# Performance work log

Hardware: AMD Instinct MI355X
Metric: run time of the kernel (lower is better)

## Reference

```python
import jax, jax.numpy as jnp
import numpy as np

N = 50000      # nodes
E = 500000     # edges
D = 128        # model dim (in_dim == out_dim)
H = 8          # heads
DH = D // H    # head dim = 16
BN_EPS = 1e-5
Z_EPS = 1e-6


def setup_inputs() -> dict:
    key = jax.random.key(0)
    ks = jax.random.split(key, 24)
    w = lambda k, shape, s=0.05: (jax.random.normal(k, shape, jnp.float32) * s)
    inp = {}
    inp['v'] = jax.random.normal(ks[0], (N, D), jnp.float32)
    inp['e'] = jax.random.normal(ks[1], (E, D), jnp.float32)
    inp['envelope'] = jax.random.uniform(ks[2], (E, 1, 1), jnp.float32)
    inp['src'] = jax.random.randint(ks[3], (E,), 0, N, jnp.int32)
    inp['dst'] = jax.random.randint(ks[4], (E,), 0, N, jnp.int32)
    # attention projections (use_bias=False)
    inp['WQ'] = w(ks[5], (D, D)); inp['WK'] = w(ks[6], (D, D))
    inp['WV'] = w(ks[7], (D, D)); inp['We'] = w(ks[8], (D, D))
    # output projections
    inp['WO_v'] = w(ks[9], (D, D)); inp['bO_v'] = jnp.zeros((D,), jnp.float32)
    inp['WO_e'] = w(ks[10], (D, D)); inp['bO_e'] = jnp.zeros((D,), jnp.float32)
    # batch-norm affine params
    inp['g1_v'] = jnp.ones((D,), jnp.float32); inp['b1_v'] = jnp.zeros((D,), jnp.float32)
    inp['g1_e'] = jnp.ones((D,), jnp.float32); inp['b1_e'] = jnp.zeros((D,), jnp.float32)
    inp['g2_v'] = jnp.ones((D,), jnp.float32); inp['b2_v'] = jnp.zeros((D,), jnp.float32)
    inp['g2_e'] = jnp.ones((D,), jnp.float32); inp['b2_e'] = jnp.zeros((D,), jnp.float32)
    # FFN weights (hidden = 2*D)
    inp['W1v'] = w(ks[11], (D, 2 * D)); inp['b1v'] = jnp.zeros((2 * D,), jnp.float32)
    inp['W2v'] = w(ks[12], (2 * D, D)); inp['b2v'] = jnp.zeros((D,), jnp.float32)
    inp['W1e'] = w(ks[13], (D, 2 * D)); inp['b1e'] = jnp.zeros((2 * D,), jnp.float32)
    inp['W2e'] = w(ks[14], (2 * D, D)); inp['b2e'] = jnp.zeros((D,), jnp.float32)
    return inp


def _batchnorm(x, g, b):
    # BatchNorm1d in training mode: biased batch stats over axis 0
    m = x.mean(0)
    var = x.var(0)
    return (x - m) * jax.lax.rsqrt(var + BN_EPS) * g + b


def _forward(v, e, envelope, src, dst,
             WQ, WK, WV, We, WO_v, bO_v, WO_e, bO_e,
             g1_v, b1_v, g1_e, b1_e,
             W1v, b1v, W2v, b2v, W1e, b1e, W2e, b2e,
             g2_v, b2_v, g2_e, b2_e):
    # --- multi-head edge attention ---
    Q = (v @ WQ).reshape(N, H, DH)
    K = (v @ WK).reshape(N, H, DH)
    V = (v @ WV).reshape(N, H, DH)
    pe = (e @ We).reshape(E, H, DH)
    # score = K[src] * Q[dst] / sqrt(Dh) * proj_e   (elementwise, per head)
    score = K[src] * Q[dst] / np.sqrt(DH).astype(np.float32) * pe  # [E,H,Dh]
    e_attn = score.reshape(E, D)                                    # e_out
    s = jnp.exp(jnp.clip(score.sum(-1, keepdims=True), -5.0, 5.0))  # [E,H,1]
    msg = V[src] * envelope * s                                     # [E,H,Dh]
    wV = jax.ops.segment_sum(msg, dst, num_segments=N)              # [N,H,Dh]
    z = jax.ops.segment_sum(s, dst, num_segments=N)                 # [N,H,1]
    v_attn = (wV / (z + Z_EPS)).reshape(N, D)
    # --- O projection + residual + batchnorm ---
    v1 = _batchnorm(v + (v_attn @ WO_v + bO_v), g1_v, b1_v)
    e1 = _batchnorm(e + (e_attn @ WO_e + bO_e), g1_e, b1_e)
    # --- FFN + residual + batchnorm ---
    v2 = _batchnorm(v1 + (jax.nn.relu(v1 @ W1v + b1v) @ W2v + b2v), g2_v, b2_v)
    e2 = _batchnorm(e1 + (jax.nn.relu(e1 @ W1e + b1e) @ W2e + b2e), g2_e, b2_e)
    return v2, e2


def reference(v, e, envelope, src, dst,
              WQ, WK, WV, We, WO_v, bO_v, WO_e, bO_e,
              g1_v, b1_v, g1_e, b1_e,
              W1v, b1v, W2v, b2v, W1e, b1e, W2e, b2e,
              g2_v, b2_v, g2_e, b2_e):
    return _forward(v, e, envelope, src, dst,
                    WQ, WK, WV, We, WO_v, bO_v, WO_e, bO_e,
                    g1_v, b1_v, g1_e, b1_e,
                    W1v, b1v, W2v, b2v, W1e, b1e, W2e, b2e,
                    g2_v, b2_v, g2_e, b2_e)
```

## Files before the change

### kernel.cpp

```cpp
#include <hip/hip_runtime.h>
#include <hip/hip_bf16.h>

#define N_NODES 50000
#define N_EDGES 500000
#define DIM 128
#define RSTRIDE 256

typedef __bf16 bf16_t;
typedef __bf16 bf16x8 __attribute__((ext_vector_type(8)));
typedef __bf16 bf16x4 __attribute__((ext_vector_type(4)));
typedef __bf16 bf16x2 __attribute__((ext_vector_type(2)));
typedef float f32x4 __attribute__((ext_vector_type(4)));

#define MFMA(a,b,c) __builtin_amdgcn_mfma_f32_16x16x32_bf16((a),(b),(c),0,0,0)

__device__ __forceinline__ int swz(int row, int kbyte){ return kbyte ^ ((row & 7) << 4); }
__device__ __forceinline__ int hswz(int row, int kbyte){ return kbyte ^ ((row & 15) << 4); }

__device__ __forceinline__ bf16x8 lds_frag(const char* s, int row, int rowb, int kbyte){
  return *(const bf16x8*)(s + row * rowb + swz(row, kbyte));
}

__device__ __forceinline__ void copy16(char* dst, const char* __restrict__ src, int bytes){
  for (int o = threadIdx.x * 16; o < bytes; o += blockDim.x * 16)
    *(f32x4*)(dst + o) = *(const f32x4*)(src + o);
}

struct WPrep {
  const float* w[10];
  int Kd[10], Nd[10], off[10], cum[10], mode[10];
};

__global__ void k_wprep(WPrep d, char* img, int total){
  for (int idx = blockIdx.x * blockDim.x + threadIdx.x; idx < total; idx += gridDim.x * blockDim.x){
    int i = 0;
#pragma unroll
    for (int j = 1; j < 10; j++) if (idx >= d.cum[j]) i = j;
    int loc = idx - d.cum[i];
    int K = d.Kd[i], N = d.Nd[i];
    int n = loc / K, k = loc - n * K;
    float val = d.w[i][(size_t)k * N + n];
    int nn = n;
    if (d.mode[i] == 1) nn = ((n & 7) << 4) | (n >> 3);
    if (d.mode[i] == 3) nn = ((n & 15) << 4) | (n >> 4);
    *(bf16_t*)(img + d.off[i] + nn * (K * 2) + swz(nn, k * 2)) = (bf16_t)val;
  }
}

__global__ void k_count(const int* __restrict__ dst, int* __restrict__ cnt){
  int i = blockIdx.x * blockDim.x + threadIdx.x;
  if (i < N_EDGES) atomicAdd(&cnt[dst[i]], 1);
}

__global__ __launch_bounds__(1024) void k_scan(const int* __restrict__ cnt,
                                               int* __restrict__ rowptr, int* __restrict__ wp){
  __shared__ int wsum[16];
  __shared__ int wpre[16];
  __shared__ int scarry;
  const int tid = threadIdx.x, lane = tid & 63, wv = tid >> 6;
  if (tid == 0) scarry = 0;
  for (int base = 0; base < N_NODES; base += 8192){
    int i0 = base + tid * 8;
    int v[8], p[8];
    int tsum = 0;
#pragma unroll
    for (int j = 0; j < 8; j++){
      int idx = i0 + j;
      v[j] = (idx < N_NODES) ? cnt[idx] : 0;
      p[j] = tsum; tsum += v[j];
    }
    int x = tsum;
#pragma unroll
    for (int off = 1; off < 64; off <<= 1){
      int t = __shfl_up(x, off);
      if (lane >= off) x += t;
    }
    if (lane == 63) wsum[wv] = x;
    __syncthreads();
    if (tid == 0){
      int run = scarry;
#pragma unroll
      for (int j = 0; j < 16; j++){ int t = wsum[j]; wpre[j] = run; run += t; }
      scarry = run;
    }
    __syncthreads();
    int texcl = wpre[wv] + x - tsum;
#pragma unroll
    for (int j = 0; j < 8; j++){
      int idx = i0 + j;
      if (idx < N_NODES){ rowptr[idx] = texcl + p[j]; wp[idx] = texcl + p[j]; }
    }
    __syncthreads();
  }
  if (tid == 0) rowptr[N_NODES] = scarry;
}

__global__ void k_fill(const int* __restrict__ dst, int* __restrict__ wp, int* __restrict__ csr){
  int i = blockIdx.x * blockDim.x + threadIdx.x;
  if (i < N_EDGES){
    int p = atomicAdd(&wp[dst[i]], 1);
    csr[p] = i;
  }
}

__global__ __launch_bounds__(512) void k_qkv(
    const float* __restrict__ v, const char* __restrict__ img,
    bf16_t* __restrict__ Q, bf16_t* __restrict__ K, bf16_t* __restrict__ V, int M)
{
  __shared__ __align__(16) char sm[65536];
  char* sX = sm;
  char* sW = sm + 32768;
  const int tid = threadIdx.x, lane = tid & 63, wave = tid >> 6;
  const int r0 = blockIdx.x * 128;
  for (int c = tid; c < 2048; c += 512){
    int row = c >> 4, kc = c & 15, grow = r0 + row;
    float f[8];
    if (grow < M){
      const float4* p = (const float4*)(v + (size_t)grow * DIM + kc * 8);
      float4 u0 = p[0], u1 = p[1];
      f[0]=u0.x; f[1]=u0.y; f[2]=u0.z; f[3]=u0.w;
      f[4]=u1.x; f[5]=u1.y; f[6]=u1.z; f[7]=u1.w;
    } else {
#pragma unroll
      for (int j=0;j<8;j++) f[j] = 0.f;
    }
    bf16x8 o;
#pragma unroll
    for (int j=0;j<8;j++) o[j] = (bf16_t)f[j];
    *(bf16x8*)(sX + row * 256 + swz(row, kc * 16)) = o;
  }
  const int rowA = wave * 16 + (lane & 15);
  const int kb0 = (lane >> 4) * 16;
  const int crow = wave*16 + (lane >> 4)*4;
  const int ccol = lane & 15;
  const f32x4 zero4 = {0.f, 0.f, 0.f, 0.f};
#pragma unroll
  for (int w3 = 0; w3 < 3; w3++){
    __syncthreads();
    copy16(sW, img + w3 * 32768, 32768);
    __syncthreads();
    f32x4 acc[8];
#pragma unroll
    for (int b=0;b<8;b++) acc[b] = zero4;
#pragma unroll
    for (int ks=0; ks<4; ks++){
      bf16x8 a = lds_frag(sX, rowA, 256, ks*64 + kb0);
#pragma unroll
      for (int nt=0; nt<8; nt++){
        int rn = nt*16 + (lane & 15);
        bf16x8 b = lds_frag(sW, rn, 256, ks*64 + kb0);
        acc[nt] = MFMA(a, b, acc[nt]);
      }
    }
    bf16_t* o = (w3 == 0) ? Q : ((w3 == 1) ? K : V);
#pragma unroll
    for (int r=0; r<4; r++){
      int grow = r0 + crow + r;
      if (grow < M){
        bf16x8 t;
#pragma unroll
        for (int nt=0; nt<8; nt++) t[nt] = (bf16_t)acc[nt][r];
        *(bf16x8*)(o + (size_t)grow * DIM + ccol*8) = t;
      }
    }
  }
}

__global__ __launch_bounds__(512, 4) void k_edge(
    const float* __restrict__ e,
    const int* __restrict__ src, const int* __restrict__ dst,
    const bf16_t* __restrict__ Qb, const bf16_t* __restrict__ Kb,
    const char* __restrict__ imgWe, const char* __restrict__ imgWo,
    const float* __restrict__ bOe,
    bf16_t* __restrict__ e1_pre, float* __restrict__ sv,
    float* __restrict__ stats, int M)
{
  __shared__ __align__(16) char sm[33792];
  char* sBuf = sm;
  float* sStats = (float*)(sm + 32768);
  const int tid = threadIdx.x, lane = tid & 63, wave = tid >> 6;
  const int r0 = blockIdx.x * 128;
  const int q = lane >> 4, ccol = lane & 15;
  const int crow = wave*16 + q*4;
  const int rowA = wave*16 + ccol;
  const int kb0 = q * 16;
  bf16x8 Kg[4], Qg[4];
#pragma unroll
  for (int r=0;r<4;r++){
    int ed = r0 + crow + r; if (ed >= M) ed = M - 1;
    int sn = src[ed], dn = dst[ed];
    Kg[r] = *(const bf16x8*)(Kb + (size_t)sn * DIM + ccol * 8);
    Qg[r] = *(const bf16x8*)(Qb + (size_t)dn * DIM + ccol * 8);
  }
  int grA = r0 + rowA; if (grA >= M) grA = M - 1;
  const f32x4* epA = (const f32x4*)(e + (size_t)grA * DIM);
  f32x4 ea[8];
#pragma unroll
  for (int ks=0; ks<4; ks++){
    ea[2*ks]   = epA[ks*8 + q*2];
    ea[2*ks+1] = epA[ks*8 + q*2 + 1];
  }
  copy16(sBuf, imgWe, 32768);
  bf16x8 eAb[4];
#pragma unroll
  for (int ks=0; ks<4; ks++){
#pragma unroll
    for (int j=0;j<4;j++){
      eAb[ks][j]   = (bf16_t)ea[2*ks][j];
      eAb[ks][4+j] = (bf16_t)ea[2*ks+1][j];
    }
  }
  __syncthreads();
  const f32x4 zero4 = {0.f,0.f,0.f,0.f};
  f32x4 pe[8];
#pragma unroll
  for (int i=0;i<8;i++) pe[i] = zero4;
#pragma unroll
  for (int ks=0; ks<4; ks++){
#pragma unroll
    for (int nt=0; nt<8; nt++){
      bf16x8 b = lds_frag(sBuf, nt*16 + ccol, 256, ks*64 + kb0);
      pe[nt] = MFMA(eAb[ks], b, pe[nt]);
    }
  }
  __syncthreads();
#pragma unroll
  for (int r=0;r<4;r++){
    int row = crow + r;
    bf16x8 t;
    float hsum = 0.f;
#pragma unroll
    for (int nt=0; nt<8; nt++){
      float sc = pe[nt][r] * 0.25f * (float)Kg[r][nt] * (float)Qg[r][nt];
      t[nt] = (bf16_t)sc;
      hsum += sc;
    }
    *(bf16x8*)(sBuf + row*256 + swz(row, ccol*16)) = t;
    float ts = hsum + __shfl_xor(hsum, 1);
    int ed = r0 + row;
    if (!(ccol & 1) && ed < M)
      sv[(size_t)ed*8 + (ccol >> 1)] = __expf(fminf(5.f, fmaxf(-5.f, ts)));
  }
  bf16x8 w2a[4];
#pragma unroll
  for (int ks=0; ks<4; ks++)
    w2a[ks] = *(const bf16x8*)(imgWo + rowA*256 + swz(rowA, ks*64 + kb0));
  __syncthreads();
  f32x4 a2[8];
#pragma unroll
  for (int i=0;i<8;i++) a2[i] = zero4;
#pragma unroll
  for (int ks=0; ks<4; ks++){
#pragma unroll
    for (int nt=0; nt<8; nt++){
      bf16x8 b = lds_frag(sBuf, nt*16 + ccol, 256, ks*64 + kb0);
      a2[nt] = MFMA(w2a[ks], b, a2[nt]);
    }
  }
  float4 bo = *(const float4*)(bOe + crow);
  float s1[4] = {0.f,0.f,0.f,0.f}, s2[4] = {0.f,0.f,0.f,0.f};
#pragma unroll
  for (int nt=0; nt<8; nt++){
    int erow = r0 + nt*16 + ccol;
    int gr = (erow < M) ? erow : (M - 1);
    f32x4 er = *(const f32x4*)(e + (size_t)gr*DIM + crow);
    float val[4];
    val[0] = a2[nt][0] + er[0] + bo.x;
    val[1] = a2[nt][1] + er[1] + bo.y;
    val[2] = a2[nt][2] + er[2] + bo.z;
    val[3] = a2[nt][3] + er[3] + bo.w;
    if (erow < M){
      bf16x4 t;
#pragma unroll
      for (int r=0;r<4;r++) t[r] = (bf16_t)val[r];
      *(bf16x4*)(e1_pre + (size_t)erow*RSTRIDE + crow) = t;
    } else {
#pragma unroll
      for (int r=0;r<4;r++) val[r] = 0.f;
    }
#pragma unroll
    for (int r=0;r<4;r++){ s1[r] += val[r]; s2[r] += val[r]*val[r]; }
  }
#pragma unroll
  for (int r=0;r<4;r++){
    s1[r] += __shfl_xor(s1[r], 1); s1[r] += __shfl_xor(s1[r], 2);
    s1[r] += __shfl_xor(s1[r], 4); s1[r] += __shfl_xor(s1[r], 8);
    s2[r] += __shfl_xor(s2[r], 1); s2[r] += __shfl_xor(s2[r], 2);
    s2[r] += __shfl_xor(s2[r], 4); s2[r] += __shfl_xor(s2[r], 8);
  }
  if (ccol == 0){
#pragma unroll
    for (int r=0;r<4;r++){
      sStats[crow + r] = s1[r];
      sStats[128 + crow + r] = s2[r];
    }
  }
  __syncthreads();
  if (tid < 256) unsafeAtomicAdd(&stats[tid], sStats[tid]);
}

__global__ __launch_bounds__(512) void k_agg(
    const int* __restrict__ rowptr, const int* __restrict__ csr,
    const int* __restrict__ src, const float* __restrict__ envl,
    const float* __restrict__ sv, const bf16_t* __restrict__ V,
    bf16_t* __restrict__ vAttn, int M)
{
  const int wave = threadIdx.x >> 6, lane = threadIdx.x & 63;
  const int n = blockIdx.x * 8 + wave;
  if (n >= M) return;
  const int beg = rowptr[n], end = rowptr[n + 1];
  const int h = lane >> 3;
  float ax = 0.f, ay = 0.f, zacc = 0.f;
  int i = beg;
  for (; i + 4 <= end; i += 4){
    int e0 = csr[i], e1 = csr[i+1], e2 = csr[i+2], e3 = csr[i+3];
    int sn0 = src[e0], sn1 = src[e1], sn2 = src[e2], sn3 = src[e3];
    float sv0 = sv[(size_t)e0*8 + h], sv1 = sv[(size_t)e1*8 + h];
    float sv2 = sv[(size_t)e2*8 + h], sv3 = sv[(size_t)e3*8 + h];
    float n0 = envl[e0], n1 = envl[e1], n2 = envl[e2], n3 = envl[e3];
    bf16x2 a0 = *(const bf16x2*)(V + (size_t)sn0 * DIM + lane * 2);
    bf16x2 a1 = *(const bf16x2*)(V + (size_t)sn1 * DIM + lane * 2);
    bf16x2 a2v = *(const bf16x2*)(V + (size_t)sn2 * DIM + lane * 2);
    bf16x2 a3 = *(const bf16x2*)(V + (size_t)sn3 * DIM + lane * 2);
    float w0 = n0*sv0, w1 = n1*sv1, w2 = n2*sv2, w3 = n3*sv3;
    ax += (float)a0[0]*w0 + (float)a1[0]*w1 + (float)a2v[0]*w2 + (float)a3[0]*w3;
    ay += (float)a0[1]*w0 + (float)a1[1]*w1 + (float)a2v[1]*w2 + (float)a3[1]*w3;
    zacc += sv0 + sv1 + sv2 + sv3;
  }
  for (; i < end; i++){
    int eid = csr[i];
    int sn = src[eid];
    float s = sv[(size_t)eid * 8 + h];
    float env = envl[eid];
    const bf16x2 vv = *(const bf16x2*)(V + (size_t)sn * DIM + lane * 2);
    float w = env * s;
    ax += (float)vv[0] * w; ay += (float)vv[1] * w;
    zacc += s;
  }
  float inv = 1.f / (zacc + 1e-6f);
  bf16x2 o; o[0] = (bf16_t)(ax * inv); o[1] = (bf16_t)(ay * inv);
  *(bf16x2*)(vAttn + (size_t)n * DIM + lane * 2) = o;
}

__global__ __launch_bounds__(512) void k_nodeout(
    const bf16_t* __restrict__ vAttn, const float* __restrict__ v,
    const char* __restrict__ imgWo, const float* __restrict__ bOv,
    bf16_t* __restrict__ v1_pre, float* __restrict__ stats, int M)
{
  __shared__ __align__(16) char sm[66560];
  char* sW = sm;
  char* sX = sm + 32768;
  float* sStats = (float*)(sm + 65536);
  const int tid = threadIdx.x, lane = tid & 63, wave = tid >> 6;
  const int r0 = blockIdx.x * 128;
  copy16(sW, imgWo, 32768);
  if (tid < 256) sStats[tid] = 0.f;
  for (int c = tid; c < 2048; c += 512){
    int row = c >> 4, kc = c & 15, grow = r0 + row;
    bf16x8 o;
    if (grow < M){
      o = *(const bf16x8*)(vAttn + (size_t)grow * DIM + kc * 8);
    } else {
#pragma unroll
      for (int j=0;j<8;j++) o[j] = (bf16_t)0.f;
    }
    *(bf16x8*)(sX + row*256 + swz(row, kc*16)) = o;
  }
  __syncthreads();
  const int rowA = wave*16 + (lane & 15);
  const int kb0 = (lane >> 4)*16;
  const f32x4 zero4 = {0.f,0.f,0.f,0.f};
  f32x4 acc[8];
#pragma unroll
  for (int i=0;i<8;i++) acc[i]=zero4;
#pragma unroll
  for (int ks=0;ks<4;ks++){
    bf16x8 a = lds_frag(sX, rowA, 256, ks*64+kb0);
#pragma unroll
    for (int nt=0;nt<8;nt++){
      int rn = nt*16 + (lane&15);
      bf16x8 b = lds_frag(sW, rn, 256, ks*64+kb0);
      acc[nt] = MFMA(a,b,acc[nt]);
    }
  }
  const int crow = wave*16 + (lane>>4)*4;
  const int ccol = lane & 15;
  float4 bo0 = *(const float4*)(bOv + ccol*8);
  float4 bo1 = *(const float4*)(bOv + ccol*8 + 4);
  float s1[8], s2[8];
#pragma unroll
  for (int j=0;j<8;j++){ s1[j]=0.f; s2[j]=0.f; }
#pragma unroll
  for (int r=0;r<4;r++){
    int grow = r0 + crow + r;
    float val[8];
    if (grow < M){
      const float4* vp = (const float4*)(v + (size_t)grow*DIM + ccol*8);
      float4 v0 = vp[0], v1 = vp[1];
      val[0]=acc[0][r]+v0.x+bo0.x; val[1]=acc[1][r]+v0.y+bo0.y;
      val[2]=acc[2][r]+v0.z+bo0.z; val[3]=acc[3][r]+v0.w+bo0.w;
      val[4]=acc[4][r]+v1.x+bo1.x; val[5]=acc[5][r]+v1.y+bo1.y;
      val[6]=acc[6][r]+v1.z+bo1.z; val[7]=acc[7][r]+v1.w+bo1.w;
      bf16x8 t;
#pragma unroll
      for (int j=0;j<8;j++) t[j] = (bf16_t)val[j];
      *(bf16x8*)(v1_pre + (size_t)grow*RSTRIDE + ccol*8) = t;
    } else {
#pragma unroll
      for (int j=0;j<8;j++) val[j]=0.f;
    }
#pragma unroll
    for (int j=0;j<8;j++){ s1[j] += val[j]; s2[j] += val[j]*val[j]; }
  }
#pragma unroll
  for (int j=0;j<8;j++){
    s1[j] += __shfl_xor(s1[j], 16); s1[j] += __shfl_xor(s1[j], 32);
    s2[j] += __shfl_xor(s2[j], 16); s2[j] += __shfl_xor(s2[j], 32);
  }
  if (lane < 16){
#pragma unroll
    for (int j=0;j<8;j++){
      atomicAdd(&sStats[ccol*8 + j], s1[j]);
      atomicAdd(&sStats[128 + ccol*8 + j], s2[j]);
    }
  }
  __syncthreads();
  if (tid < 256) unsafeAtomicAdd(&stats[tid], sStats[tid]);
}

struct FinArgs { const float* st; const float* g; const float* b; float* ss; float invM; };

__global__ void k_finstats(FinArgs a0, FinArgs a1){
  FinArgs a = (blockIdx.x == 0) ? a0 : a1;
  int c = threadIdx.x;
  float mean = a.st[c] * a.invM;
  float var  = a.st[128 + c] * a.invM - mean * mean;
  float scl  = a.g[c] * rsqrtf(var + 1e-5f);
  a.ss[c] = scl;
  a.ss[128 + c] = a.b[c] - mean * scl;
}

__global__ __launch_bounds__(512, 4) void k_ffn(
    bf16_t* __restrict__ xio, const float* __restrict__ ss1,
    const char* __restrict__ img1, const float* __restrict__ b1,
    const char* __restrict__ img2, const float* __restrict__ b2,
    float* __restrict__ stats2, int M)
{
  __shared__ __align__(16) char sm[66560];
  char* sA = sm;
  char* sB = sm + 32768;
  float* sStats = (float*)(sm + 65536);
  const int tid = threadIdx.x, lane = tid & 63, wave = tid >> 6;
  const int r0 = blockIdx.x * 128;
  const int rowA = wave*16 + (lane & 15);
  const int q = lane >> 4;
  const int kb0 = q * 16;
  const int crow = wave*16 + q*4;
  const int ccol = lane & 15;
  const f32x4 zero4 = {0.f,0.f,0.f,0.f};

  float4 sc0 = *(const float4*)(ss1 + ccol*8);
  float4 sc1 = *(const float4*)(ss1 + ccol*8 + 4);
  float4 sh0 = *(const float4*)(ss1 + 128 + ccol*8);
  float4 sh1 = *(const float4*)(ss1 + 128 + ccol*8 + 4);
  const float4* bq = (const float4*)(b1 + ccol * 16);
  float4 bq0 = bq[0], bq1 = bq[1], bq2 = bq[2], bq3 = bq[3];

  copy16(sB, img1, 32768);
  if (tid < 256) sStats[tid] = 0.f;
  int grA = r0 + rowA; if (grA >= M) grA = M - 1;
  const bf16_t* xrow = xio + (size_t)grA * RSTRIDE;
  bf16x8 araw[4];
#pragma unroll
  for (int ks=0; ks<4; ks++)
    araw[ks] = *(const bf16x8*)(xrow + ks*32 + q*8);
  bf16x8 xres[4];
#pragma unroll
  for (int r = 0; r < 4; r++){
    int grow = r0 + crow + r;
    bf16x8 o;
    if (grow < M){
      bf16x8 u = *(const bf16x8*)(xio + (size_t)grow*RSTRIDE + ccol*8);
      o[0]=(bf16_t)((float)u[0]*sc0.x+sh0.x); o[1]=(bf16_t)((float)u[1]*sc0.y+sh0.y);
      o[2]=(bf16_t)((float)u[2]*sc0.z+sh0.z); o[3]=(bf16_t)((float)u[3]*sc0.w+sh0.w);
      o[4]=(bf16_t)((float)u[4]*sc1.x+sh1.x); o[5]=(bf16_t)((float)u[5]*sc1.y+sh1.y);
      o[6]=(bf16_t)((float)u[6]*sc1.z+sh1.z); o[7]=(bf16_t)((float)u[7]*sc1.w+sh1.w);
    } else {
#pragma unroll
      for (int j=0;j<8;j++) o[j]=(bf16_t)0.f;
    }
    xres[r] = o;
  }
  bf16x8 xAb[4];
#pragma unroll
  for (int ks=0; ks<4; ks++){
    const f32x4* sp = (const f32x4*)(ss1 + ks*32 + q*8);
    const f32x4* hp = (const f32x4*)(ss1 + 128 + ks*32 + q*8);
    f32x4 s0 = sp[0], s1v = sp[1], h0 = hp[0], h1 = hp[1];
#pragma unroll
    for (int j=0;j<4;j++){
      xAb[ks][j]   = (bf16_t)((float)araw[ks][j]  *s0[j]  + h0[j]);
      xAb[ks][4+j] = (bf16_t)((float)araw[ks][4+j]*s1v[j] + h1[j]);
    }
  }
  __syncthreads();

  bf16x8 hreg[8];
  f32x4 wbuf[4];

#pragma unroll
  for (int i=0;i<4;i++) wbuf[i] = *(const f32x4*)(img1 + 32768 + tid*16 + i*8192);
  {
    f32x4 acc[8];
#pragma unroll
    for (int i=0;i<8;i++) acc[i]=zero4;
#pragma unroll
    for (int ks=0;ks<4;ks++){
#pragma unroll
      for (int nt=0;nt<8;nt++){
        int rn = nt*16 + (lane&15);
        bf16x8 b = lds_frag(sB, rn, 256, ks*64+kb0);
        acc[nt] = MFMA(xAb[ks], b, acc[nt]);
      }
    }
#pragma unroll
    for (int r=0;r<4;r++){
      bf16x8 t;
      t[0]=(bf16_t)fmaxf(acc[0][r]+bq0.x,0.f); t[1]=(bf16_t)fmaxf(acc[1][r]+bq0.y,0.f);
      t[2]=(bf16_t)fmaxf(acc[2][r]+bq0.z,0.f); t[3]=(bf16_t)fmaxf(acc[3][r]+bq0.w,0.f);
      t[4]=(bf16_t)fmaxf(acc[4][r]+bq1.x,0.f); t[5]=(bf16_t)fmaxf(acc[5][r]+bq1.y,0.f);
      t[6]=(bf16_t)fmaxf(acc[6][r]+bq1.z,0.f); t[7]=(bf16_t)fmaxf(acc[7][r]+bq1.w,0.f);
      hreg[r] = t;
    }
  }
  __syncthreads();
#pragma unroll
  for (int i=0;i<4;i++) *(f32x4*)(sB + tid*16 + i*8192) = wbuf[i];
  __syncthreads();
#pragma unroll
  for (int i=0;i<4;i++){
    int o = tid*16 + i*8192;
    wbuf[i] = *(const f32x4*)(img2 + (o >> 8)*512 + (o & 255));
  }
  {
    f32x4 acc[8];
#pragma unroll
    for (int i=0;i<8;i++) acc[i]=zero4;
#pragma unroll
    for (int ks=0;ks<4;ks++){
#pragma unroll
      for (int nt=0;nt<8;nt++){
        int rn = nt*16 + (lane&15);
        bf16x8 b = lds_frag(sB, rn, 256, ks*64+kb0);
        acc[nt] = MFMA(xAb[ks], b, acc[nt]);
      }
    }
#pragma unroll
    for (int r=0;r<4;r++){
      bf16x8 t;
      t[0]=(bf16_t)fmaxf(acc[0][r]+bq2.x,0.f); t[1]=(bf16_t)fmaxf(acc[1][r]+bq2.y,0.f);
      t[2]=(bf16_t)fmaxf(acc[2][r]+bq2.z,0.f); t[3]=(bf16_t)fmaxf(acc[3][r]+bq2.w,0.f);
      t[4]=(bf16_t)fmaxf(acc[4][r]+bq3.x,0.f); t[5]=(bf16_t)fmaxf(acc[5][r]+bq3.y,0.f);
      t[6]=(bf16_t)fmaxf(acc[6][r]+bq3.z,0.f); t[7]=(bf16_t)fmaxf(acc[7][r]+bq3.w,0.f);
      hreg[4+r] = t;
    }
  }
  __syncthreads();

  f32x4 o2[8];
#pragma unroll
  for (int i=0;i<8;i++) o2[i]=zero4;

#pragma unroll
  for (int half = 0; half < 2; half++){
    if ((ccol >> 3) == half){
      int cb = (ccol & 7) * 32;
#pragma unroll
      for (int r=0;r<4;r++){
        int row = crow + r;
        *(bf16x8*)(sA + row*256 + hswz(row, cb))      = hreg[r];
        *(bf16x8*)(sA + row*256 + hswz(row, cb + 16)) = hreg[4+r];
      }
    }
#pragma unroll
    for (int i=0;i<4;i++) *(f32x4*)(sB + tid*16 + i*8192) = wbuf[i];
    __syncthreads();
    if (half == 0){
#pragma unroll
      for (int i=0;i<4;i++){
        int o = tid*16 + i*8192;
        wbuf[i] = *(const f32x4*)(img2 + (o >> 8)*512 + 256 + (o & 255));
      }
    }
#pragma unroll
    for (int ks=0;ks<4;ks++){
      bf16x8 a = *(const bf16x8*)(sA + rowA*256 + hswz(rowA, ks*64+kb0));
#pragma unroll
      for (int nt=0;nt<8;nt++){
        int rn = nt*16 + (lane&15);
        bf16x8 b = lds_frag(sB, rn, 256, ks*64+kb0);
        o2[nt] = MFMA(a,b,o2[nt]);
      }
    }
    __syncthreads();
  }

  float4 b20 = *(const float4*)(b2 + ccol*8);
  float4 b21 = *(const float4*)(b2 + ccol*8 + 4);
  float s1[8], s2[8];
#pragma unroll
  for (int j=0;j<8;j++){ s1[j]=0.f; s2[j]=0.f; }
#pragma unroll
  for (int r=0;r<4;r++){
    int grow = r0 + crow + r;
    float val[8];
    val[0]=(float)xres[r][0]+o2[0][r]+b20.x; val[1]=(float)xres[r][1]+o2[1][r]+b20.y;
    val[2]=(float)xres[r][2]+o2[2][r]+b20.z; val[3]=(float)xres[r][3]+o2[3][r]+b20.w;
    val[4]=(float)xres[r][4]+o2[4][r]+b21.x; val[5]=(float)xres[r][5]+o2[5][r]+b21.y;
    val[6]=(float)xres[r][6]+o2[6][r]+b21.z; val[7]=(float)xres[r][7]+o2[7][r]+b21.w;
    if (grow < M){
      bf16x8 t;
#pragma unroll
      for (int j=0;j<8;j++) t[j] = (bf16_t)val[j];
      *(bf16x8*)(xio + (size_t)grow*RSTRIDE + ccol*8) = t;
    } else {
#pragma unroll
      for (int j=0;j<8;j++) val[j]=0.f;
    }
#pragma unroll
    for (int j=0;j<8;j++){ s1[j] += val[j]; s2[j] += val[j]*val[j]; }
  }
#pragma unroll
  for (int j=0;j<8;j++){
    s1[j] += __shfl_xor(s1[j], 16); s1[j] += __shfl_xor(s1[j], 32);
    s2[j] += __shfl_xor(s2[j], 16); s2[j] += __shfl_xor(s2[j], 32);
  }
  if (lane < 16){
#pragma unroll
    for (int j=0;j<8;j++){
      atomicAdd(&sStats[ccol*8 + j], s1[j]);
      atomicAdd(&sStats[128 + ccol*8 + j], s2[j]);
    }
  }
  __syncthreads();
  if (tid < 256) unsafeAtomicAdd(&stats2[tid], sStats[tid]);
}

struct NormP { const float* st; const float* g; const float* bn; float invM; };

__global__ __launch_bounds__(256) void k_norm2(
    char* __restrict__ xv, char* __restrict__ xe,
    NormP pv, NormP pe, long long nv, long long ne)
{
  __shared__ float sSS[512];
  const int tid = threadIdx.x;
  {
    int side = tid >> 7, c = tid & 127;
    NormP pp = side ? pe : pv;
    float mean = pp.st[c] * pp.invM;
    float var  = pp.st[128 + c] * pp.invM - mean * mean;
    float scl  = pp.g[c] * rsqrtf(var + 1e-5f);
    sSS[side*256 + c] = scl;
    sSS[side*256 + 128 + c] = pp.bn[c] - mean * scl;
  }
  __syncthreads();
  long long tv = nv * 16, total = tv + ne * 16;
  for (long long g = (long long)blockIdx.x * blockDim.x + tid; g < total;
       g += (long long)gridDim.x * blockDim.x){
    bool isv = g < tv;
    char* base = isv ? xv : xe;
    const float* ss = isv ? sSS : (sSS + 256);
    long long gg = isv ? g : g - tv;
    long long row = gg >> 4;
    int c = (int)(gg & 15);
    bf16x8 u = *(const bf16x8*)(base + row * 512 + c * 16);
    int c0 = c * 8;
    float4 o0, o1;
    o0.x = (float)u[0]*ss[c0+0] + ss[128+c0+0];
    o0.y = (float)u[1]*ss[c0+1] + ss[128+c0+1];
    o0.z = (float)u[2]*ss[c0+2] + ss[128+c0+2];
    o0.w = (float)u[3]*ss[c0+3] + ss[128+c0+3];
    o1.x = (float)u[4]*ss[c0+4] + ss[128+c0+4];
    o1.y = (float)u[5]*ss[c0+5] + ss[128+c0+5];
    o1.z = (float)u[6]*ss[c0+6] + ss[128+c0+6];
    o1.w = (float)u[7]*ss[c0+7] + ss[128+c0+7];
    float4* dp = (float4*)(base + row * 512 + c * 32);
    dp[0] = o0; dp[1] = o1;
  }
}

extern "C" void kernel_launch(void* const* d_in, const int* in_sizes, int n_in,
                              void* d_out, int out_size, void* d_ws, size_t ws_size,
                              hipStream_t stream)
{
  const float* v    = (const float*)d_in[0];
  const float* e    = (const float*)d_in[1];
  const float* envl = (const float*)d_in[2];
  const int*   src  = (const int*)d_in[3];
  const int*   dst  = (const int*)d_in[4];
  const float* bOv  = (const float*)d_in[10];
  const float* bOe  = (const float*)d_in[12];
  const float* g1v  = (const float*)d_in[13];
  const float* b1vn = (const float*)d_in[14];
  const float* g1e  = (const float*)d_in[15];
  const float* b1en = (const float*)d_in[16];
  const float* g2v  = (const float*)d_in[17];
  const float* b2vn = (const float*)d_in[18];
  const float* g2e  = (const float*)d_in[19];
  const float* b2en = (const float*)d_in[20];
  const float* b1vf = (const float*)d_in[22];
  const float* b2vf = (const float*)d_in[24];
  const float* b1ef = (const float*)d_in[26];
  const float* b2ef = (const float*)d_in[28];

  float* out_v = (float*)d_out;
  float* out_e = out_v + (size_t)N_NODES * DIM;
  bf16_t* v1b = (bf16_t*)out_v;
  bf16_t* e1b = (bf16_t*)out_e;

  char* ws = (char*)d_ws;
  const size_t IMG_OFF = 0;
  const size_t QB_OFF  = 458752;
  const size_t KB_OFF  = QB_OFF  + 12800000;
  const size_t VB_OFF  = KB_OFF  + 12800000;
  const size_t VA_OFF  = VB_OFF  + 12800000;
  const size_t SV_OFF  = VA_OFF  + 12800000;
  const size_t CSR_OFF = SV_OFF  + 16000000;
  const size_t RP_OFF  = CSR_OFF + 2000000;
  const size_t WP_OFF  = RP_OFF  + 200016;
  const size_t CNT_OFF = WP_OFF  + 200000;
  const size_t ST_OFF  = CNT_OFF + 200000;
  const size_t SS_OFF  = ST_OFF  + 4096;

  char*   img   = ws + IMG_OFF;
  bf16_t* Qb    = (bf16_t*)(ws + QB_OFF);
  bf16_t* Kb    = (bf16_t*)(ws + KB_OFF);
  bf16_t* Vb    = (bf16_t*)(ws + VB_OFF);
  bf16_t* vAttn = (bf16_t*)(ws + VA_OFF);
  float*  svp   = (float*)(ws + SV_OFF);
  int*    csr   = (int*)(ws + CSR_OFF);
  int*    rowp  = (int*)(ws + RP_OFF);
  int*    wpp   = (int*)(ws + WP_OFF);
  int*    cnt   = (int*)(ws + CNT_OFF);
  float*  st    = (float*)(ws + ST_OFF);
  float*  ssb   = (float*)(ws + SS_OFF);
  float* st_e1 = st;        float* st_v1 = st + 256;
  float* st_v2 = st + 512;  float* st_e2 = st + 768;
  float* ss_v1 = ssb;       float* ss_e1 = ssb + 256;

  (void)hipMemsetAsync(ws + CNT_OFF, 0, 200000 + 4096, stream);

  WPrep wp;
  const int wid[10]   = {5,6,7,8,9,11,21,23,25,27};
  const int Ks[10]    = {128,128,128,128,128,128,128,256,128,256};
  const int Ns[10]    = {128,128,128,128,128,128,256,128,256,128};
  const int modes[10] = {1,1,1,1,1,0,3,1,3,1};
  int cum = 0, off = 0;
  for (int i = 0; i < 10; i++){
    wp.w[i] = (const float*)d_in[wid[i]];
    wp.Kd[i] = Ks[i]; wp.Nd[i] = Ns[i];
    wp.off[i] = off; wp.cum[i] = cum; wp.mode[i] = modes[i];
    off += Ks[i]*Ns[i]*2; cum += Ks[i]*Ns[i];
  }
  k_wprep<<<896, 256, 0, stream>>>(wp, img, cum);

  k_count<<<1954, 256, 0, stream>>>(dst, cnt);
  k_scan<<<1, 1024, 0, stream>>>(cnt, rowp, wpp);
  k_fill<<<1954, 256, 0, stream>>>(dst, wpp, csr);

  k_qkv<<<391, 512, 0, stream>>>(v, img, Qb, Kb, Vb, N_NODES);

  k_edge<<<3907, 512, 0, stream>>>(e, src, dst, Qb, Kb,
                                   img + 98304 , img + 163840 , bOe,
                                   e1b, svp, st_e1, N_EDGES);

  k_agg<<<6250, 512, 0, stream>>>(rowp, csr, src, envl, svp, Vb, vAttn, N_NODES);

  k_nodeout<<<391, 512, 0, stream>>>(vAttn, v, img + 131072 , bOv,
                                     v1b, st_v1, N_NODES);

  {
    FinArgs fv{st_v1, g1v, b1vn, ss_v1, 1.f / N_NODES};
    FinArgs fe{st_e1, g1e, b1en, ss_e1, 1.f / N_EDGES};
    k_finstats<<<2, 128, 0, stream>>>(fv, fe);
  }

  k_ffn<<<391, 512, 0, stream>>>(v1b, ss_v1, img + 196608 , b1vf,
                                 img + 262144 , b2vf, st_v2, N_NODES);
  k_ffn<<<3907, 512, 0, stream>>>(e1b, ss_e1, img + 327680 , b1ef,
                                  img + 393216 , b2ef, st_e2, N_EDGES);

  NormP npv{st_v2, g2v, b2vn, 1.f / N_NODES};
  NormP npe{st_e2, g2e, b2en, 1.f / N_EDGES};
  k_norm2<<<4096, 256, 0, stream>>>((char*)out_v, (char*)out_e, npv, npe,
                                    (long long)N_NODES, (long long)N_EDGES);
}
```

Before: 712.0 us.

## Transpose FFN second GEMM to halve LDS and raise occupancy

The FFN kernel now computes the second GEMM transposed. W2 fragments are read straight from global memory as the A operand, and the hidden activations are staged in LDS as the B operand. This drops the separate weight and activation LDS buffers to a single 32KB buffer and raises the launch-bounds occupancy hint from 4 to 6. The residual is re-read in column-oriented form instead of being held in registers, and the stats reduction switches to shuffles over the 16 lanes. The weight-prep mode for W2 changes to match. The risks are extra global reads of W2 per block and narrower 8-byte residual accesses.

```diff
diff --git a/kernel.cpp b/kernel.cpp
--- a/kernel.cpp
+++ b/kernel.cpp
@@ -440,57 +440,30 @@
   a.ss[128 + c] = a.b[c] - mean * scl;
 }
 
-__global__ __launch_bounds__(512, 4) void k_ffn(
+__global__ __launch_bounds__(512, 6) void k_ffn(
     bf16_t* __restrict__ xio, const float* __restrict__ ss1,
     const char* __restrict__ img1, const float* __restrict__ b1,
     const char* __restrict__ img2, const float* __restrict__ b2,
     float* __restrict__ stats2, int M)
 {
-  __shared__ __align__(16) char sm[66560];
-  char* sA = sm;
-  char* sB = sm + 32768;
-  float* sStats = (float*)(sm + 65536);
+  __shared__ __align__(16) char sm[33792];
+  char* sBuf = sm;
+  float* sStats = (float*)(sm + 32768);
   const int tid = threadIdx.x, lane = tid & 63, wave = tid >> 6;
   const int r0 = blockIdx.x * 128;
-  const int rowA = wave*16 + (lane & 15);
-  const int q = lane >> 4;
+  const int q = lane >> 4, ccol = lane & 15;
   const int kb0 = q * 16;
   const int crow = wave*16 + q*4;
-  const int ccol = lane & 15;
+  const int rowA = wave*16 + ccol;
   const f32x4 zero4 = {0.f,0.f,0.f,0.f};
 
-  float4 sc0 = *(const float4*)(ss1 + ccol*8);
-  float4 sc1 = *(const float4*)(ss1 + ccol*8 + 4);
-  float4 sh0 = *(const float4*)(ss1 + 128 + ccol*8);
-  float4 sh1 = *(const float4*)(ss1 + 128 + ccol*8 + 4);
-  const float4* bq = (const float4*)(b1 + ccol * 16);
-  float4 bq0 = bq[0], bq1 = bq[1], bq2 = bq[2], bq3 = bq[3];
-
-  copy16(sB, img1, 32768);
-  if (tid < 256) sStats[tid] = 0.f;
+  copy16(sBuf, img1, 32768);
   int grA = r0 + rowA; if (grA >= M) grA = M - 1;
   const bf16_t* xrow = xio + (size_t)grA * RSTRIDE;
   bf16x8 araw[4];
 #pragma unroll
   for (int ks=0; ks<4; ks++)
     araw[ks] = *(const bf16x8*)(xrow + ks*32 + q*8);
-  bf16x8 xres[4];
-#pragma unroll
-  for (int r = 0; r < 4; r++){
-    int grow = r0 + crow + r;
-    bf16x8 o;
-    if (grow < M){
-      bf16x8 u = *(const bf16x8*)(xio + (size_t)grow*RSTRIDE + ccol*8);
-      o[0]=(bf16_t)((float)u[0]*sc0.x+sh0.x); o[1]=(bf16_t)((float)u[1]*sc0.y+sh0.y);
-      o[2]=(bf16_t)((float)u[2]*sc0.z+sh0.z); o[3]=(bf16_t)((float)u[3]*sc0.w+sh0.w);
-      o[4]=(bf16_t)((float)u[4]*sc1.x+sh1.x); o[5]=(bf16_t)((float)u[5]*sc1.y+sh1.y);
-      o[6]=(bf16_t)((float)u[6]*sc1.z+sh1.z); o[7]=(bf16_t)((float)u[7]*sc1.w+sh1.w);
-    } else {
-#pragma unroll
-      for (int j=0;j<8;j++) o[j]=(bf16_t)0.f;
-    }
-    xres[r] = o;
-  }
   bf16x8 xAb[4];
 #pragma unroll
   for (int ks=0; ks<4; ks++){
@@ -505,12 +478,13 @@
   }
   __syncthreads();
 
-  bf16x8 hreg[8];
+  bf16x8 hreg0[4], hreg1[4];
   f32x4 wbuf[4];
-
 #pragma unroll
   for (int i=0;i<4;i++) wbuf[i] = *(const f32x4*)(img1 + 32768 + tid*16 + i*8192);
   {
+    float4 bq0 = *(const float4*)(b1 + ccol*16);
+    float4 bq1 = *(const float4*)(b1 + ccol*16 + 4);
     f32x4 acc[8];
 #pragma unroll
     for (int i=0;i<8;i++) acc[i]=zero4;
@@ -518,8 +492,7 @@
     for (int ks=0;ks<4;ks++){
 #pragma unroll
       for (int nt=0;nt<8;nt++){
-        int rn = nt*16 + (lane&15);
-        bf16x8 b = lds_frag(sB, rn, 256, ks*64+kb0);
+        bf16x8 b = lds_frag(sBuf, nt*16 + ccol, 256, ks*64+kb0);
         acc[nt] = MFMA(xAb[ks], b, acc[nt]);
       }
     }
@@ -530,19 +503,16 @@
       t[2]=(bf16_t)fmaxf(acc[2][r]+bq0.z,0.f); t[3]=(bf16_t)fmaxf(acc[3][r]+bq0.w,0.f);
       t[4]=(bf16_t)fmaxf(acc[4][r]+bq1.x,0.f); t[5]=(bf16_t)fmaxf(acc[5][r]+bq1.y,0.f);
       t[6]=(bf16_t)fmaxf(acc[6][r]+bq1.z,0.f); t[7]=(bf16_t)fmaxf(acc[7][r]+bq1.w,0.f);
-      hreg[r] = t;
-    }
-  }
-  __syncthreads();
-#pragma unroll
-  for (int i=0;i<4;i++) *(f32x4*)(sB + tid*16 + i*8192) = wbuf[i];
-  __syncthreads();
-#pragma unroll
-  for (int i=0;i<4;i++){
-    int o = tid*16 + i*8192;
-    wbuf[i] = *(const f32x4*)(img2 + (o >> 8)*512 + (o & 255));
-  }
+      hreg0[r] = t;
+    }
+  }
+  __syncthreads();
+#pragma unroll
+  for (int i=0;i<4;i++) *(f32x4*)(sBuf + tid*16 + i*8192) = wbuf[i];
+  __syncthreads();
   {
+    float4 bq2 = *(const float4*)(b1 + ccol*16 + 8);
+    float4 bq3 = *(const float4*)(b1 + ccol*16 + 12);
     f32x4 acc[8];
 #pragma unroll
     for (int i=0;i<8;i++) acc[i]=zero4;
@@ -550,8 +520,7 @@
     for (int ks=0;ks<4;ks++){
 #pragma unroll
       for (int nt=0;nt<8;nt++){
-        int rn = nt*16 + (lane&15);
-        bf16x8 b = lds_frag(sB, rn, 256, ks*64+kb0);
+        bf16x8 b = lds_frag(sBuf, nt*16 + ccol, 256, ks*64+kb0);
         acc[nt] = MFMA(xAb[ks], b, acc[nt]);
       }
     }
@@ -562,7 +531,18 @@
       t[2]=(bf16_t)fmaxf(acc[2][r]+bq2.z,0.f); t[3]=(bf16_t)fmaxf(acc[3][r]+bq2.w,0.f);
       t[4]=(bf16_t)fmaxf(acc[4][r]+bq3.x,0.f); t[5]=(bf16_t)fmaxf(acc[5][r]+bq3.y,0.f);
       t[6]=(bf16_t)fmaxf(acc[6][r]+bq3.z,0.f); t[7]=(bf16_t)fmaxf(acc[7][r]+bq3.w,0.f);
-      hreg[4+r] = t;
+      hreg1[r] = t;
+    }
+  }
+  __syncthreads();
+
+  if ((ccol >> 3) == 0){
+    int cb = (ccol & 7) * 32;
+#pragma unroll
+    for (int r=0;r<4;r++){
+      int row = crow + r;
+      *(bf16x8*)(sBuf + row*256 + hswz(row, cb))      = hreg0[r];
+      *(bf16x8*)(sBuf + row*256 + hswz(row, cb + 16)) = hreg1[r];
     }
   }
   __syncthreads();
@@ -570,76 +550,86 @@
   f32x4 o2[8];
 #pragma unroll
   for (int i=0;i<8;i++) o2[i]=zero4;
-
-#pragma unroll
-  for (int half = 0; half < 2; half++){
-    if ((ccol >> 3) == half){
-      int cb = (ccol & 7) * 32;
-#pragma unroll
-      for (int r=0;r<4;r++){
-        int row = crow + r;
-        *(bf16x8*)(sA + row*256 + hswz(row, cb))      = hreg[r];
-        *(bf16x8*)(sA + row*256 + hswz(row, cb + 16)) = hreg[4+r];
+  {
+    bf16x8 w2a[4];
+#pragma unroll
+    for (int ks=0; ks<4; ks++)
+      w2a[ks] = *(const bf16x8*)(img2 + (size_t)rowA*512 + swz(rowA, ks*64 + kb0));
+#pragma unroll
+    for (int ks=0; ks<4; ks++){
+#pragma unroll
+      for (int nt=0; nt<8; nt++){
+        int m = nt*16 + ccol;
+        bf16x8 b = *(const bf16x8*)(sBuf + m*256 + hswz(m, ks*64 + kb0));
+        o2[nt] = MFMA(w2a[ks], b, o2[nt]);
       }
     }
-#pragma unroll
-    for (int i=0;i<4;i++) *(f32x4*)(sB + tid*16 + i*8192) = wbuf[i];
-    __syncthreads();
-    if (half == 0){
-#pragma unroll
-      for (int i=0;i<4;i++){
-        int o = tid*16 + i*8192;
-        wbuf[i] = *(const f32x4*)(img2 + (o >> 8)*512 + 256 + (o & 255));
+  }
+  __syncthreads();
+  if ((ccol >> 3) == 1){
+    int cb = (ccol & 7) * 32;
+#pragma unroll
+    for (int r=0;r<4;r++){
+      int row = crow + r;
+      *(bf16x8*)(sBuf + row*256 + hswz(row, cb))      = hreg0[r];
+      *(bf16x8*)(sBuf + row*256 + hswz(row, cb + 16)) = hreg1[r];
+    }
+  }
+  __syncthreads();
+  {
+    bf16x8 w2a[4];
+#pragma unroll
+    for (int ks=0; ks<4; ks++)
+      w2a[ks] = *(const bf16x8*)(img2 + (size_t)rowA*512 + swz(rowA, 256 + ks*64 + kb0));
+#pragma unroll
+    for (int ks=0; ks<4; ks++){
+#pragma unroll
+      for (int nt=0; nt<8; nt++){
+        int m = nt*16 + ccol;
+        bf16x8 b = *(const bf16x8*)(sBuf + m*256 + hswz(m, ks*64 + kb0));
+        o2[nt] = MFMA(w2a[ks], b, o2[nt]);
       }
     }
-#pragma unroll
-    for (int ks=0;ks<4;ks++){
-      bf16x8 a = *(const bf16x8*)(sA + rowA*256 + hswz(rowA, ks*64+kb0));
-#pragma unroll
-      for (int nt=0;nt<8;nt++){
-        int rn = nt*16 + (lane&15);
-        bf16x8 b = lds_frag(sB, rn, 256, ks*64+kb0);
-        o2[nt] = MFMA(a,b,o2[nt]);
-      }
-    }
-    __syncthreads();
-  }
-
-  float4 b20 = *(const float4*)(b2 + ccol*8);
-  float4 b21 = *(const float4*)(b2 + ccol*8 + 4);
-  float s1[8], s2[8];
-#pragma unroll
-  for (int j=0;j<8;j++){ s1[j]=0.f; s2[j]=0.f; }
+  }
+
+  float4 ssc = *(const float4*)(ss1 + crow);
+  float4 ssh = *(const float4*)(ss1 + 128 + crow);
+  float4 b2v = *(const float4*)(b2 + crow);
+  float s1[4] = {0.f,0.f,0.f,0.f}, s2[4] = {0.f,0.f,0.f,0.f};
+#pragma unroll
+  for (int nt=0; nt<8; nt++){
+    int erow = r0 + nt*16 + ccol;
+    int gr = (erow < M) ? erow : (M - 1);
+    bf16x4 u = *(const bf16x4*)(xio + (size_t)gr*RSTRIDE + crow);
+    float val[4];
+    val[0] = (float)u[0]*ssc.x + ssh.x + o2[nt][0] + b2v.x;
+    val[1] = (float)u[1]*ssc.y + ssh.y + o2[nt][1] + b2v.y;
+    val[2] = (float)u[2]*ssc.z + ssh.z + o2[nt][2] + b2v.z;
+    val[3] = (float)u[3]*ssc.w + ssh.w + o2[nt][3] + b2v.w;
+    if (erow < M){
+      bf16x4 t;
+#pragma unroll
+      for (int r=0;r<4;r++) t[r] = (bf16_t)val[r];
+      *(bf16x4*)(xio + (size_t)erow*RSTRIDE + crow) = t;
+    } else {
+#pragma unroll
+      for (int r=0;r<4;r++) val[r] = 0.f;
+    }
+#pragma unroll
+    for (int r=0;r<4;r++){ s1[r] += val[r]; s2[r] += val[r]*val[r]; }
+  }
 #pragma unroll
   for (int r=0;r<4;r++){
-    int grow = r0 + crow + r;
-    float val[8];
-    val[0]=(float)xres[r][0]+o2[0][r]+b20.x; val[1]=(float)xres[r][1]+o2[1][r]+b20.y;
-    val[2]=(float)xres[r][2]+o2[2][r]+b20.z; val[3]=(float)xres[r][3]+o2[3][r]+b20.w;
-    val[4]=(float)xres[r][4]+o2[4][r]+b21.x; val[5]=(float)xres[r][5]+o2[5][r]+b21.y;
-    val[6]=(float)xres[r][6]+o2[6][r]+b21.z; val[7]=(float)xres[r][7]+o2[7][r]+b21.w;
-    if (grow < M){
-      bf16x8 t;
-#pragma unroll
-      for (int j=0;j<8;j++) t[j] = (bf16_t)val[j];
-      *(bf16x8*)(xio + (size_t)grow*RSTRIDE + ccol*8) = t;
-    } else {
-#pragma unroll
-      for (int j=0;j<8;j++) val[j]=0.f;
-    }
-#pragma unroll
-    for (int j=0;j<8;j++){ s1[j] += val[j]; s2[j] += val[j]*val[j]; }
-  }
-#pragma unroll
-  for (int j=0;j<8;j++){
-    s1[j] += __shfl_xor(s1[j], 16); s1[j] += __shfl_xor(s1[j], 32);
-    s2[j] += __shfl_xor(s2[j], 16); s2[j] += __shfl_xor(s2[j], 32);
-  }
-  if (lane < 16){
-#pragma unroll
-    for (int j=0;j<8;j++){
-      atomicAdd(&sStats[ccol*8 + j], s1[j]);
-      atomicAdd(&sStats[128 + ccol*8 + j], s2[j]);
+    s1[r] += __shfl_xor(s1[r], 1); s1[r] += __shfl_xor(s1[r], 2);
+    s1[r] += __shfl_xor(s1[r], 4); s1[r] += __shfl_xor(s1[r], 8);
+    s2[r] += __shfl_xor(s2[r], 1); s2[r] += __shfl_xor(s2[r], 2);
+    s2[r] += __shfl_xor(s2[r], 4); s2[r] += __shfl_xor(s2[r], 8);
+  }
+  if (ccol == 0){
+#pragma unroll
+    for (int r=0;r<4;r++){
+      sStats[crow + r] = s1[r];
+      sStats[128 + crow + r] = s2[r];
     }
   }
   __syncthreads();
@@ -754,7 +744,7 @@
   const int wid[10]   = {5,6,7,8,9,11,21,23,25,27};
   const int Ks[10]    = {128,128,128,128,128,128,128,256,128,256};
   const int Ns[10]    = {128,128,128,128,128,128,256,128,256,128};
-  const int modes[10] = {1,1,1,1,1,0,3,1,3,1};
+  const int modes[10] = {1,1,1,1,1,0,3,0,3,0};
   int cum = 0, off = 0;
   for (int i = 0; i < 10; i++){
     wp.w[i] = (const float*)d_in[wid[i]];
```

Result: slower. 759.4 us (+6.7%).
